# Kernel tuning notes

Hardware: AMD Instinct MI355X
Metric: run time of the kernel (lower is better)

Reference implementation:

```python
import jax, jax.numpy as jnp
import numpy as np

SCALE = 1.0

def setup_inputs() -> dict:
    key = jax.random.key(0)
    k1, k2 = jax.random.split(key)
    features = jax.random.normal(k1, (16, 512, 128, 128), dtype=jnp.float32)
    probs = jax.random.normal(k2, (16, 19, 128, 128), dtype=jnp.float32)
    return {"features": features, "probs": probs}

def reference(features, probs):
    B, K, H, W = probs.shape
    C = features.shape[1]
    p = probs.reshape(B, K, H * W)               # [B, K, HW]
    f = features.reshape(B, C, H * W)            # [B, C, HW]
    attn = jax.nn.softmax(SCALE * p, axis=2)     # softmax over spatial dim
    # ocr_context[b, k, c] = sum_hw attn[b,k,hw] * f[b,c,hw]
    ctx = jnp.einsum('bks,bcs->bkc', attn, f)    # [B, K, C]
    return jnp.transpose(ctx, (0, 2, 1))[..., None]  # [B, C, K, 1]
```

## Files before the change

### kernel.cpp

```cpp
#include <hip/hip_runtime.h>
#include <math.h>

#define BATCH 16
#define KCLS  19
#define CCH   512
#define HW    16384

#define KSPLIT 16
#define KB     (HW / KSPLIT)
#define BK     64
#define NCHUNK (KB / BK)
#define NT     128

typedef __attribute__((ext_vector_type(8))) short  short8;
typedef __attribute__((ext_vector_type(4))) float  floatx4;

static __device__ __forceinline__ ushort f2bf(float x) {
  unsigned u = __float_as_uint(x);
  return (ushort)((u + 0x7FFFu + ((u >> 16) & 1u)) >> 16);
}

__global__ __launch_bounds__(256) void softmax_stats_kernel(
    const float* __restrict__ probs, float* __restrict__ stats) {
  const int bk = blockIdx.x;
  const float4* row = (const float4*)(probs + (size_t)bk * HW);
  const int tid  = threadIdx.x;
  const int lane = tid & 63;
  const int wave = tid >> 6;
  __shared__ float red[4];

  float m = -1e30f;
  for (int i = tid; i < HW / 4; i += 256) {
    float4 v = row[i];
    m = fmaxf(m, fmaxf(fmaxf(v.x, v.y), fmaxf(v.z, v.w)));
  }
  for (int off = 32; off > 0; off >>= 1) m = fmaxf(m, __shfl_xor(m, off));
  if (lane == 0) red[wave] = m;
  __syncthreads();
  m = fmaxf(fmaxf(red[0], red[1]), fmaxf(red[2], red[3]));

  float s = 0.f;
  for (int i = tid; i < HW / 4; i += 256) {
    float4 v = row[i];
    s += __expf(v.x - m) + __expf(v.y - m) + __expf(v.z - m) + __expf(v.w - m);
  }
  for (int off = 32; off > 0; off >>= 1) s += __shfl_xor(s, off);
  __syncthreads();
  if (lane == 0) red[wave] = s;
  __syncthreads();
  if (tid == 0) {
    float total = red[0] + red[1] + red[2] + red[3];
    stats[2 * bk]     = m;
    stats[2 * bk + 1] = 1.0f / total;
  }
}

__global__ __launch_bounds__(256, 2) void gather_mfma(
    const float* __restrict__ feat, const float* __restrict__ probs,
    const float* __restrict__ stats, float* __restrict__ out) {
  __shared__ __align__(16) short A[2][32][BK];
  __shared__ __align__(16) short F[2][NT][BK];

  const int bid = blockIdx.x;
  const int b   = bid & 15;
  const int r1  = bid >> 4;
  const int ct  = r1 & 3;
  const int ks  = r1 >> 2;
  const int k0  = ks * KB;

  const int tid  = threadIdx.x;
  const int wave = tid >> 6;
  const int lane = tid & 63;

  const float* fbase = feat  + ((size_t)(b * CCH + ct * NT)) * HW + k0;
  const float* pbase = probs + ((size_t)b * KCLS) * HW + k0;

  const int  prow = tid >> 3, pg = tid & 7;
  const bool pact = (tid < KCLS * 8);
  float pm = 0.f, pinv = 0.f;
  if (pact) {
    pm   = stats[2 * (b * KCLS + prow)];
    pinv = stats[2 * (b * KCLS + prow) + 1];
  }

  floatx4 acc00 = {0,0,0,0}, acc01 = {0,0,0,0}, acc10 = {0,0,0,0}, acc11 = {0,0,0,0};

  float4 fA0, fB0, fA1, fB1, fA2, fB2, fA3, fB3;
  float4 pA, pB;

#define LOADC(c)                                                                \
  {                                                                             \
    const float* p0 = fbase + (size_t)((tid +   0) >> 3) * HW + (c) * BK + ((tid & 7) * 8); \
    const float* p1 = fbase + (size_t)((tid + 256) >> 3) * HW + (c) * BK + ((tid & 7) * 8); \
    const float* p2 = fbase + (size_t)((tid + 512) >> 3) * HW + (c) * BK + ((tid & 7) * 8); \
    const float* p3 = fbase + (size_t)((tid + 768) >> 3) * HW + (c) * BK + ((tid & 7) * 8); \
    fA0 = *(const float4*)p0;  fB0 = *(const float4*)(p0 + 4);                  \
    fA1 = *(const float4*)p1;  fB1 = *(const float4*)(p1 + 4);                  \
    fA2 = *(const float4*)p2;  fB2 = *(const float4*)(p2 + 4);                  \
    fA3 = *(const float4*)p3;  fB3 = *(const float4*)(p3 + 4);                  \
    if (pact) {                                                                 \
      const float* q = pbase + (size_t)prow * HW + (c) * BK + pg * 8;           \
      pA = *(const float4*)q;  pB = *(const float4*)(q + 4);                    \
    }                                                                           \
  }

#define WR1(buf, it, va, vb)                                                    \
  {                                                                             \
    int i  = tid + 256 * (it);                                                  \
    int ch = i >> 3, g = i & 7;                                                 \
    short8 v;                                                                   \
    v[0]=(short)f2bf(va.x); v[1]=(short)f2bf(va.y); v[2]=(short)f2bf(va.z); v[3]=(short)f2bf(va.w); \
    v[4]=(short)f2bf(vb.x); v[5]=(short)f2bf(vb.y); v[6]=(short)f2bf(vb.z); v[7]=(short)f2bf(vb.w); \
    *(short8*)((char*)&F[buf][0][0] + ch * 128 + ((g ^ (ch & 7)) * 16)) = v;    \
  }

#define WRITEC(buf)                                                             \
  {                                                                             \
    WR1(buf, 0, fA0, fB0)  WR1(buf, 1, fA1, fB1)                                \
    WR1(buf, 2, fA2, fB2)  WR1(buf, 3, fA3, fB3)                                \
    if (pact) {                                                                 \
      short8 v;                                                                 \
      v[0]=(short)f2bf(__expf(pA.x - pm) * pinv); v[1]=(short)f2bf(__expf(pA.y - pm) * pinv); \
      v[2]=(short)f2bf(__expf(pA.z - pm) * pinv); v[3]=(short)f2bf(__expf(pA.w - pm) * pinv); \
      v[4]=(short)f2bf(__expf(pB.x - pm) * pinv); v[5]=(short)f2bf(__expf(pB.y - pm) * pinv); \
      v[6]=(short)f2bf(__expf(pB.z - pm) * pinv); v[7]=(short)f2bf(__expf(pB.w - pm) * pinv); \
      *(short8*)((char*)&A[buf][0][0] + prow * 128 + ((pg ^ (prow & 7)) * 16)) = v; \
    }                                                                           \
  }

#define GEMMC(buf)                                                              \
  {                                                                             \
    _Pragma("unroll")                                                           \
    for (int kt = 0; kt < 2; kt++) {                                            \
      const int gA  = kt * 4 + (lane >> 4);                                     \
      const int rm0 = lane & 15;                                                \
      const int rm1 = 16 + rm0;                                                 \
      const int ch0 = wave * 32 + (lane & 15);                                  \
      const int ch1 = ch0 + 16;                                                 \
      short8 a0 = *(const short8*)((char*)&A[buf][0][0] + rm0 * 128 + ((gA ^ (rm0 & 7)) * 16)); \
      short8 a1 = *(const short8*)((char*)&A[buf][0][0] + rm1 * 128 + ((gA ^ (rm1 & 7)) * 16)); \
      short8 b0 = *(const short8*)((char*)&F[buf][0][0] + ch0 * 128 + ((gA ^ (ch0 & 7)) * 16)); \
      short8 b1 = *(const short8*)((char*)&F[buf][0][0] + ch1 * 128 + ((gA ^ (ch1 & 7)) * 16)); \
      acc00 = __builtin_amdgcn_mfma_f32_16x16x32_bf16(a0, b0, acc00, 0, 0, 0);  \
      acc01 = __builtin_amdgcn_mfma_f32_16x16x32_bf16(a0, b1, acc01, 0, 0, 0);  \
      acc10 = __builtin_amdgcn_mfma_f32_16x16x32_bf16(a1, b0, acc10, 0, 0, 0);  \
      acc11 = __builtin_amdgcn_mfma_f32_16x16x32_bf16(a1, b1, acc11, 0, 0, 0);  \
    }                                                                           \
  }

  LOADC(0);
  WRITEC(0);
  __syncthreads();

  for (int c = 0; c < NCHUNK; c++) {
    if (c + 1 < NCHUNK) LOADC(c + 1);
    GEMMC(c & 1);
    if (c + 1 < NCHUNK) WRITEC((c + 1) & 1);
    __syncthreads();
  }

  {
    const int chb = ct * NT + wave * 32;
    const int rb  = (lane >> 4) * 4;
    const int cl  = lane & 15;
    #pragma unroll
    for (int j = 0; j < 4; j++) {
      int row = rb + j;
      atomicAdd(&out[((size_t)(b * CCH + chb + cl))      * KCLS + row], acc00[j]);
      atomicAdd(&out[((size_t)(b * CCH + chb + 16 + cl)) * KCLS + row], acc01[j]);
      int row1 = 16 + row;
      if (row1 < KCLS) {
        atomicAdd(&out[((size_t)(b * CCH + chb + cl))      * KCLS + row1], acc10[j]);
        atomicAdd(&out[((size_t)(b * CCH + chb + 16 + cl)) * KCLS + row1], acc11[j]);
      }
    }
  }
#undef LOADC
#undef WR1
#undef WRITEC
#undef GEMMC
}

extern "C" void kernel_launch(void* const* d_in, const int* in_sizes, int n_in,
                              void* d_out, int out_size, void* d_ws, size_t ws_size,
                              hipStream_t stream) {
  const float* feat  = (const float*)d_in[0];
  const float* probs = (const float*)d_in[1];
  float* out   = (float*)d_out;
  float* stats = (float*)d_ws;

  hipMemsetAsync(d_out, 0, (size_t)out_size * sizeof(float), stream);

  softmax_stats_kernel<<<BATCH * KCLS, 256, 0, stream>>>(probs, stats);
  gather_mfma<<<BATCH * 4 * KSPLIT, 256, 0, stream>>>(feat, probs, stats, out);
}
```

Baseline: 148.8 us.

## Stream features to LDS via direct global_load_lds and replace atomics with split-K reduce

Feature tiles are now copied straight from global memory into LDS as fp32 with the async global_load_lds path, and converted to bf16 only when each wave reads its MFMA operands. This takes the register round-trip and the separate conversion-store stage off the load path. The atomicAdd epilogue and the output memset are replaced by per-split partial buffers plus a separate reduction kernel. In exchange, LDS use doubles, so occupancy drops to one block per CU. The change also adds a partials write/read pass and an extra kernel launch.

After: 139.3 us. -6.4%, faster.

```diff
diff --git a/kernel.cpp b/kernel.cpp
--- a/kernel.cpp
+++ b/kernel.cpp
@@ -11,13 +11,27 @@
 #define BK     64
 #define NCHUNK (KB / BK)
 #define NT     128
+#define KPAD   20
+#define BCN    (BATCH * CCH)
 
 typedef __attribute__((ext_vector_type(8))) short  short8;
 typedef __attribute__((ext_vector_type(4))) float  floatx4;
+
+typedef __attribute__((address_space(3))) void*        lds_ptr_t;
+typedef const __attribute__((address_space(1))) void*  gbl_ptr_t;
 
 static __device__ __forceinline__ ushort f2bf(float x) {
   unsigned u = __float_as_uint(x);
   return (ushort)((u + 0x7FFFu + ((u >> 16) & 1u)) >> 16);
+}
+
+static __device__ __forceinline__ short8 pack8(float4 a, float4 b) {
+  short8 v;
+  v[0] = (short)f2bf(a.x); v[1] = (short)f2bf(a.y);
+  v[2] = (short)f2bf(a.z); v[3] = (short)f2bf(a.w);
+  v[4] = (short)f2bf(b.x); v[5] = (short)f2bf(b.y);
+  v[6] = (short)f2bf(b.z); v[7] = (short)f2bf(b.w);
+  return v;
 }
 
 __global__ __launch_bounds__(256) void softmax_stats_kernel(
@@ -55,11 +69,11 @@
   }
 }
 
-__global__ __launch_bounds__(256, 2) void gather_mfma(
+__global__ __launch_bounds__(256, 1) void gather_mfma(
     const float* __restrict__ feat, const float* __restrict__ probs,
-    const float* __restrict__ stats, float* __restrict__ out) {
-  __shared__ __align__(16) short A[2][32][BK];
-  __shared__ __align__(16) short F[2][NT][BK];
+    const float* __restrict__ stats, float* __restrict__ part) {
+  __shared__ __align__(16) float Fs[2][NT][BK];
+  __shared__ __align__(16) short As[2][32][BK];
 
   const int bid = blockIdx.x;
   const int b   = bid & 15;
@@ -84,52 +98,45 @@
   }
 
   floatx4 acc00 = {0,0,0,0}, acc01 = {0,0,0,0}, acc10 = {0,0,0,0}, acc11 = {0,0,0,0};
-
-  float4 fA0, fB0, fA1, fB1, fA2, fB2, fA3, fB3;
   float4 pA, pB;
 
-#define LOADC(c)                                                                \
+#define DMA_CHUNK(buf, c)                                                       \
   {                                                                             \
-    const float* p0 = fbase + (size_t)((tid +   0) >> 3) * HW + (c) * BK + ((tid & 7) * 8); \
-    const float* p1 = fbase + (size_t)((tid + 256) >> 3) * HW + (c) * BK + ((tid & 7) * 8); \
-    const float* p2 = fbase + (size_t)((tid + 512) >> 3) * HW + (c) * BK + ((tid & 7) * 8); \
-    const float* p3 = fbase + (size_t)((tid + 768) >> 3) * HW + (c) * BK + ((tid & 7) * 8); \
-    fA0 = *(const float4*)p0;  fB0 = *(const float4*)(p0 + 4);                  \
-    fA1 = *(const float4*)p1;  fB1 = *(const float4*)(p1 + 4);                  \
-    fA2 = *(const float4*)p2;  fB2 = *(const float4*)(p2 + 4);                  \
-    fA3 = *(const float4*)p3;  fB3 = *(const float4*)(p3 + 4);                  \
-    if (pact) {                                                                 \
-      const float* q = pbase + (size_t)prow * HW + (c) * BK + pg * 8;           \
-      pA = *(const float4*)q;  pB = *(const float4*)(q + 4);                    \
+    char* lb = ((char*)Fs) + (buf) * 32768 + wave * 8192;                       \
+    _Pragma("unroll")                                                           \
+    for (int i = 0; i < 8; i++) {                                               \
+      int ch = wave * 32 + i * 4 + (lane >> 4);                                 \
+      const float* src = fbase + (size_t)ch * HW + (c) * BK                     \
+                         + (((lane & 15) ^ (ch & 7)) << 2);                     \
+      __builtin_amdgcn_global_load_lds((gbl_ptr_t)src,                          \
+                                       (lds_ptr_t)(lb + i * 1024), 16, 0, 0);   \
     }                                                                           \
   }
 
-#define WR1(buf, it, va, vb)                                                    \
-  {                                                                             \
-    int i  = tid + 256 * (it);                                                  \
-    int ch = i >> 3, g = i & 7;                                                 \
+#define PLOAD(c)                                                                \
+  if (pact) {                                                                   \
+    const float* q = pbase + (size_t)prow * HW + (c) * BK + pg * 8;             \
+    pA = *(const float4*)q;  pB = *(const float4*)(q + 4);                      \
+  }
+
+#define PSTAGE(buf)                                                             \
+  if (pact) {                                                                   \
     short8 v;                                                                   \
-    v[0]=(short)f2bf(va.x); v[1]=(short)f2bf(va.y); v[2]=(short)f2bf(va.z); v[3]=(short)f2bf(va.w); \
-    v[4]=(short)f2bf(vb.x); v[5]=(short)f2bf(vb.y); v[6]=(short)f2bf(vb.z); v[7]=(short)f2bf(vb.w); \
-    *(short8*)((char*)&F[buf][0][0] + ch * 128 + ((g ^ (ch & 7)) * 16)) = v;    \
-  }
-
-#define WRITEC(buf)                                                             \
-  {                                                                             \
-    WR1(buf, 0, fA0, fB0)  WR1(buf, 1, fA1, fB1)                                \
-    WR1(buf, 2, fA2, fB2)  WR1(buf, 3, fA3, fB3)                                \
-    if (pact) {                                                                 \
-      short8 v;                                                                 \
-      v[0]=(short)f2bf(__expf(pA.x - pm) * pinv); v[1]=(short)f2bf(__expf(pA.y - pm) * pinv); \
-      v[2]=(short)f2bf(__expf(pA.z - pm) * pinv); v[3]=(short)f2bf(__expf(pA.w - pm) * pinv); \
-      v[4]=(short)f2bf(__expf(pB.x - pm) * pinv); v[5]=(short)f2bf(__expf(pB.y - pm) * pinv); \
-      v[6]=(short)f2bf(__expf(pB.z - pm) * pinv); v[7]=(short)f2bf(__expf(pB.w - pm) * pinv); \
-      *(short8*)((char*)&A[buf][0][0] + prow * 128 + ((pg ^ (prow & 7)) * 16)) = v; \
-    }                                                                           \
+    v[0] = (short)f2bf(__expf(pA.x - pm) * pinv);                               \
+    v[1] = (short)f2bf(__expf(pA.y - pm) * pinv);                               \
+    v[2] = (short)f2bf(__expf(pA.z - pm) * pinv);                               \
+    v[3] = (short)f2bf(__expf(pA.w - pm) * pinv);                               \
+    v[4] = (short)f2bf(__expf(pB.x - pm) * pinv);                               \
+    v[5] = (short)f2bf(__expf(pB.y - pm) * pinv);                               \
+    v[6] = (short)f2bf(__expf(pB.z - pm) * pinv);                               \
+    v[7] = (short)f2bf(__expf(pB.w - pm) * pinv);                               \
+    *(short8*)((char*)As + (buf) * 4096 + prow * 128 + ((pg ^ (prow & 7)) << 4)) = v; \
   }
 
 #define GEMMC(buf)                                                              \
   {                                                                             \
+    const char* Ab = (const char*)As + (buf) * 4096;                            \
+    const char* Fb = (const char*)Fs + (buf) * 32768;                           \
     _Pragma("unroll")                                                           \
     for (int kt = 0; kt < 2; kt++) {                                            \
       const int gA  = kt * 4 + (lane >> 4);                                     \
@@ -137,10 +144,14 @@
       const int rm1 = 16 + rm0;                                                 \
       const int ch0 = wave * 32 + (lane & 15);                                  \
       const int ch1 = ch0 + 16;                                                 \
-      short8 a0 = *(const short8*)((char*)&A[buf][0][0] + rm0 * 128 + ((gA ^ (rm0 & 7)) * 16)); \
-      short8 a1 = *(const short8*)((char*)&A[buf][0][0] + rm1 * 128 + ((gA ^ (rm1 & 7)) * 16)); \
-      short8 b0 = *(const short8*)((char*)&F[buf][0][0] + ch0 * 128 + ((gA ^ (ch0 & 7)) * 16)); \
-      short8 b1 = *(const short8*)((char*)&F[buf][0][0] + ch1 * 128 + ((gA ^ (ch1 & 7)) * 16)); \
+      short8 a0 = *(const short8*)(Ab + rm0 * 128 + ((gA ^ (rm0 & 7)) << 4));   \
+      short8 a1 = *(const short8*)(Ab + rm1 * 128 + ((gA ^ (rm1 & 7)) << 4));   \
+      float4 b0lo = *(const float4*)(Fb + ch0 * 256 + (((2 * gA)     ^ (ch0 & 7)) << 4)); \
+      float4 b0hi = *(const float4*)(Fb + ch0 * 256 + (((2 * gA + 1) ^ (ch0 & 7)) << 4)); \
+      float4 b1lo = *(const float4*)(Fb + ch1 * 256 + (((2 * gA)     ^ (ch1 & 7)) << 4)); \
+      float4 b1hi = *(const float4*)(Fb + ch1 * 256 + (((2 * gA + 1) ^ (ch1 & 7)) << 4)); \
+      short8 b0 = pack8(b0lo, b0hi);                                            \
+      short8 b1 = pack8(b1lo, b1hi);                                            \
       acc00 = __builtin_amdgcn_mfma_f32_16x16x32_bf16(a0, b0, acc00, 0, 0, 0);  \
       acc01 = __builtin_amdgcn_mfma_f32_16x16x32_bf16(a0, b1, acc01, 0, 0, 0);  \
       acc10 = __builtin_amdgcn_mfma_f32_16x16x32_bf16(a1, b0, acc10, 0, 0, 0);  \
@@ -148,37 +159,51 @@
     }                                                                           \
   }
 
-  LOADC(0);
-  WRITEC(0);
+  DMA_CHUNK(0, 0);
+  PLOAD(0);
+  PSTAGE(0);
   __syncthreads();
 
   for (int c = 0; c < NCHUNK; c++) {
-    if (c + 1 < NCHUNK) LOADC(c + 1);
-    GEMMC(c & 1);
-    if (c + 1 < NCHUNK) WRITEC((c + 1) & 1);
+    const int cur = c & 1, nxt = cur ^ 1;
+    if (c + 1 < NCHUNK) { DMA_CHUNK(nxt, c + 1); PLOAD(c + 1); }
+    GEMMC(cur);
+    if (c + 1 < NCHUNK) PSTAGE(nxt);
     __syncthreads();
   }
 
   {
     const int chb = ct * NT + wave * 32;
+    const int cl  = lane & 15;
     const int rb  = (lane >> 4) * 4;
-    const int cl  = lane & 15;
+    size_t bc0 = (size_t)b * CCH + chb + cl;
+    size_t bc1 = bc0 + 16;
+    float* p0 = part + ((size_t)ks * BCN + bc0) * KPAD + rb;
+    float* p1 = part + ((size_t)ks * BCN + bc1) * KPAD + rb;
+    *(float4*)p0 = *(float4*)&acc00;
+    *(float4*)p1 = *(float4*)&acc01;
+    if (rb == 0) {
+      *(float4*)(p0 + 16) = *(float4*)&acc10;
+      *(float4*)(p1 + 16) = *(float4*)&acc11;
+    }
+  }
+#undef DMA_CHUNK
+#undef PLOAD
+#undef PSTAGE
+#undef GEMMC
+}
+
+__global__ __launch_bounds__(256) void reduce_kernel(
+    const float* __restrict__ part, float* __restrict__ out) {
+  const int gid = blockIdx.x * 256 + threadIdx.x;
+  const int bc = gid / KPAD, r = gid - bc * KPAD;
+  if (r < KCLS) {
+    float s = 0.f;
     #pragma unroll
-    for (int j = 0; j < 4; j++) {
-      int row = rb + j;
-      atomicAdd(&out[((size_t)(b * CCH + chb + cl))      * KCLS + row], acc00[j]);
-      atomicAdd(&out[((size_t)(b * CCH + chb + 16 + cl)) * KCLS + row], acc01[j]);
-      int row1 = 16 + row;
-      if (row1 < KCLS) {
-        atomicAdd(&out[((size_t)(b * CCH + chb + cl))      * KCLS + row1], acc10[j]);
-        atomicAdd(&out[((size_t)(b * CCH + chb + 16 + cl)) * KCLS + row1], acc11[j]);
-      }
-    }
-  }
-#undef LOADC
-#undef WR1
-#undef WRITEC
-#undef GEMMC
+    for (int k = 0; k < KSPLIT; k++)
+      s += part[(size_t)k * (BCN * KPAD) + gid];
+    out[(size_t)bc * KCLS + r] = s;
+  }
 }
 
 extern "C" void kernel_launch(void* const* d_in, const int* in_sizes, int n_in,
@@ -188,9 +213,9 @@
   const float* probs = (const float*)d_in[1];
   float* out   = (float*)d_out;
   float* stats = (float*)d_ws;
-
-  hipMemsetAsync(d_out, 0, (size_t)out_size * sizeof(float), stream);
+  float* part  = (float*)((char*)d_ws + 4096);
 
   softmax_stats_kernel<<<BATCH * KCLS, 256, 0, stream>>>(probs, stats);
-  gather_mfma<<<BATCH * 4 * KSPLIT, 256, 0, stream>>>(feat, probs, stats, out);
-}
+  gather_mfma<<<BATCH * 4 * KSPLIT, 256, 0, stream>>>(feat, probs, stats, part);
+  reduce_kernel<<<(BCN * KPAD) / 256, 256, 0, stream>>>(part, out);
+}
```
